# Performance work log

Hardware: AMD Instinct MI355X
Metric: run time of the kernel (lower is better)

Reference implementation:

```python
import jax, jax.numpy as jnp
import numpy as np

B, C, N, T = 16, 32, 1024, 128
R = 10  # low-rank bottleneck of W1/W2


def setup_inputs() -> dict:
    key = jax.random.key(0)
    k1, k2, k3, k4 = jax.random.split(key, 4)
    x = jax.random.normal(k1, (B, C, N, T), dtype=jnp.float32)
    W1 = jax.random.normal(k2, (R, N), dtype=jnp.float32) * 0.05
    W2 = jax.random.normal(k3, (R, N), dtype=jnp.float32) * 0.05
    alpha = jax.random.normal(k4, (C,), dtype=jnp.float32) * 0.1
    return {"x": x, "W1": W1, "W2": W2, "alpha": alpha}


def reference(x, W1, W2, alpha):
    # k = q = einsum('bint,i->btn', x, alpha): contract channels -> [B, T, N]
    k = jnp.einsum('bcnt,c->btn', x, alpha)
    # low-rank bilinear scores: (k @ W1^T) @ (k @ W2^T)^T -> [B, T, T]
    kw1 = jnp.einsum('btn,rn->btr', k, W1)   # [B, T, R]
    qw2 = jnp.einsum('btn,rn->btr', k, W2)   # [B, T, R]
    scores = jnp.einsum('btr,bsr->bts', kw1, qw2)  # [B, T, T]
    att = jax.nn.softmax(scores, axis=-1)
    # weighted sum over time: einsum('bti,bcni->bcnt', att, x)
    return jnp.einsum('bts,bcns->bcnt', att, x)
```

## Files before the change

kernel.cpp:

```cpp
#include <hip/hip_runtime.h>
#include <hip/hip_bf16.h>


#define B_ 16
#define C_ 32
#define N_ 1024
#define T_ 128
#define R_ 10

typedef __bf16 bf16x8 __attribute__((ext_vector_type(8)));
typedef __bf16 bf16x4 __attribute__((ext_vector_type(4)));
typedef float f32x4 __attribute__((ext_vector_type(4)));

__device__ __forceinline__ void lds_barrier() {
    asm volatile("s_waitcnt lgkmcnt(0)" ::: "memory");
    __builtin_amdgcn_s_barrier();
    asm volatile("" ::: "memory");
}

__global__ __launch_bounds__(256) void k_reduce_c(const float* __restrict__ x,
                                                  const float* __restrict__ alpha,
                                                  float* __restrict__ k) {
    int bid = blockIdx.x;
    int b   = bid >> 7;
    int nc  = bid & 127;
    int tid = threadIdx.x;
    int nl  = tid >> 5;
    int lc  = tid & 31;
    int n   = nc * 8 + nl;
    const float4* xb = reinterpret_cast<const float4*>(
        x + ((size_t)(b * C_) * N_ + n) * T_) + lc;
    float4 acc = {0.f, 0.f, 0.f, 0.f};
    #pragma unroll 8
    for (int c = 0; c < C_; ++c) {
        float a = alpha[c];
        float4 v = xb[(size_t)c * (N_ * T_ / 4)];
        acc.x += a * v.x; acc.y += a * v.y; acc.z += a * v.z; acc.w += a * v.w;
    }
    reinterpret_cast<float4*>(k + ((size_t)b * N_ + n) * T_)[lc] = acc;
}

__global__ __launch_bounds__(128) void kw_partial2(const float* __restrict__ k,
                                                   const float* __restrict__ W1,
                                                   const float* __restrict__ W2,
                                                   float* __restrict__ p1,
                                                   float* __restrict__ p2) {
    __shared__ float wl[32][20];
    int bid = blockIdx.x;
    int b   = bid >> 5;
    int ch  = bid & 31;
    int n0  = ch * 32;
    int t   = threadIdx.x;
    for (int i = t; i < 32 * 20; i += 128) {
        int nl = i & 31, q = i >> 5;
        wl[nl][q] = (q < 10) ? W1[q * N_ + n0 + nl] : W2[(q - 10) * N_ + n0 + nl];
    }
    __syncthreads();
    float a1[R_] = {}, a2[R_] = {};
    const float* kb = k + ((size_t)b * N_ + n0) * T_ + t;
    #pragma unroll 2
    for (int g = 0; g < 4; ++g) {
        float kv[8];
        #pragma unroll
        for (int j = 0; j < 8; ++j) kv[j] = kb[(g * 8 + j) * T_];
        #pragma unroll
        for (int j = 0; j < 8; ++j) {
            int nl = g * 8 + j;
            #pragma unroll
            for (int r = 0; r < R_; ++r) {
                a1[r] += kv[j] * wl[nl][r];
                a2[r] += kv[j] * wl[nl][10 + r];
            }
        }
    }
    #pragma unroll
    for (int r = 0; r < R_; ++r) {
        size_t o = (((size_t)b * R_ + r) * 32 + ch) * T_ + t;
        p1[o] = a1[r];
        p2[o] = a2[r];
    }
}

__global__ __launch_bounds__(128) void scores_softmax3(const float* __restrict__ p1,
                                                       const float* __restrict__ p2,
                                                       __bf16* __restrict__ att) {
    __shared__ __align__(16) float kw1s[T_][12];
    __shared__ __align__(16) float kw2s[T_][12];
    __shared__ float sc[T_][T_ + 1];
    int b = blockIdx.x;
    int t = threadIdx.x;
    #pragma unroll
    for (int r = 0; r < R_; ++r) {
        float s1 = 0.f, s2 = 0.f;
        const float* q1 = p1 + (((size_t)b * R_ + r) * 32) * T_ + t;
        const float* q2 = p2 + (((size_t)b * R_ + r) * 32) * T_ + t;
        #pragma unroll 4
        for (int ch = 0; ch < 32; ++ch) { s1 += q1[ch * T_]; s2 += q2[ch * T_]; }
        kw1s[t][r] = s1; kw2s[t][r] = s2;
    }
    __syncthreads();
    float myw[R_];
    #pragma unroll
    for (int r = 0; r < R_; ++r) myw[r] = kw1s[t][r];
    float mx = -1e30f;
    for (int s = 0; s < T_; ++s) {
        float wv[12];
        const float4* qr = reinterpret_cast<const float4*>(&kw2s[s][0]);
        #pragma unroll
        for (int q = 0; q < 3; ++q) *reinterpret_cast<float4*>(&wv[q * 4]) = qr[q];
        float v = 0.f;
        #pragma unroll
        for (int r = 0; r < R_; ++r) v += myw[r] * wv[r];
        sc[t][s] = v;
        mx = fmaxf(mx, v);
    }
    float sum = 0.f;
    for (int s = 0; s < T_; ++s) {
        float e = __expf(sc[t][s] - mx);
        sc[t][s] = e;
        sum += e;
    }
    float inv = 1.0f / sum;
    __bf16* arow = att + ((size_t)b * T_ + t) * T_;
    for (int s8 = 0; s8 < T_; s8 += 8) {
        bf16x8 hv;
        #pragma unroll
        for (int q = 0; q < 8; ++q) hv[q] = (__bf16)(sc[t][s8 + q] * inv);
        *reinterpret_cast<bf16x8*>(arow + s8) = hv;
    }
}

__global__ __launch_bounds__(256, 2) void out_gemm4nt(const float* __restrict__ x,
                                                      const __bf16* __restrict__ att,
                                                      float* __restrict__ out) {
    __shared__ __align__(16) __bf16 attl[T_][T_];
    __shared__ __align__(16) __bf16 xsl[2][64][T_];
    int bid = blockIdx.x;
    int sg  = bid & 3;
    int c   = (bid >> 2) & 31;
    int b   = bid >> 7;
    int tid = threadIdx.x;
    char* attb = (char*)&attl[0][0];
    size_t slab0 = ((size_t)(b * C_ + c) * N_ + (sg * 4) * 64) * T_;

    const uint4* ga = reinterpret_cast<const uint4*>(att + (size_t)b * T_ * T_);
    uint4 ar[8];
    #pragma unroll
    for (int i = 0; i < 8; ++i) ar[i] = ga[i * 256 + tid];
    const f32x4* gx0 = reinterpret_cast<const f32x4*>(x + slab0);
    f32x4 xr[8];
    #pragma unroll
    for (int j = 0; j < 8; ++j) xr[j] = __builtin_nontemporal_load(&gx0[j * 256 + tid]);
    #pragma unroll
    for (int i = 0; i < 8; ++i) {
        int e = i * 256 + tid, row = e >> 4;
        int bc = ((e & 15) * 16) ^ ((row & 7) << 4);
        *reinterpret_cast<uint4*>(attb + row * 256 + bc) = ar[i];
    }
    {
        char* xb0 = (char*)&xsl[0][0][0];
        #pragma unroll
        for (int j = 0; j < 8; ++j) {
            int e = j * 256 + tid, row = e >> 5;
            bf16x4 hv = {(__bf16)xr[j][0], (__bf16)xr[j][1], (__bf16)xr[j][2], (__bf16)xr[j][3]};
            *reinterpret_cast<bf16x4*>(xb0 + row * 256 + (((e & 31) * 8) ^ ((row & 7) << 4))) = hv;
        }
    }
    lds_barrier();

    int wave = tid >> 6, lane = tid & 63;
    int r16 = lane & 15, g = lane >> 4;
    int wt = wave & 1, wn = wave >> 1;
    int swz = (r16 & 7) << 4;

    #pragma unroll
    for (int i = 0; i < 4; ++i) {
        f32x4 xn[8];
        if (i < 3) {
            const f32x4* gxn = reinterpret_cast<const f32x4*>(
                x + slab0 + ((size_t)(i + 1) * 64) * T_);
            #pragma unroll
            for (int j = 0; j < 8; ++j) xn[j] = __builtin_nontemporal_load(&gxn[j * 256 + tid]);
        }
        const char* xbb = (const char*)&xsl[i & 1][0][0];
        f32x4 acc[2][4] = {};
        #pragma unroll
        for (int ks = 0; ks < 4; ++ks) {
            int kc = ks * 64 + g * 16;
            bf16x8 a[4], bx[2];
            #pragma unroll
            for (int tt = 0; tt < 4; ++tt)
                a[tt] = *reinterpret_cast<const bf16x8*>(
                    attb + (wt * 64 + tt * 16 + r16) * 256 + (kc ^ swz));
            #pragma unroll
            for (int nn = 0; nn < 2; ++nn)
                bx[nn] = *reinterpret_cast<const bf16x8*>(
                    xbb + (wn * 32 + nn * 16 + r16) * 256 + (kc ^ swz));
            #pragma unroll
            for (int nn = 0; nn < 2; ++nn)
                #pragma unroll
                for (int tt = 0; tt < 4; ++tt)
                    acc[nn][tt] = __builtin_amdgcn_mfma_f32_16x16x32_bf16(
                        a[tt], bx[nn], acc[nn][tt], 0, 0, 0);
        }
        float* o = out + slab0 + ((size_t)i * 64) * T_;
        #pragma unroll
        for (int nn = 0; nn < 2; ++nn) {
            int n_l = wn * 32 + nn * 16 + r16;
            #pragma unroll
            for (int tt = 0; tt < 4; ++tt)
                __builtin_nontemporal_store(acc[nn][tt],
                    reinterpret_cast<f32x4*>(
                        o + (size_t)n_l * T_ + (wt * 64 + tt * 16 + g * 4)));
        }
        if (i < 3) {
            char* xw = (char*)&xsl[(i + 1) & 1][0][0];
            #pragma unroll
            for (int j = 0; j < 8; ++j) {
                int e = j * 256 + tid, row = e >> 5;
                bf16x4 hv = {(__bf16)xn[j][0], (__bf16)xn[j][1],
                             (__bf16)xn[j][2], (__bf16)xn[j][3]};
                *reinterpret_cast<bf16x4*>(
                    xw + row * 256 + (((e & 31) * 8) ^ ((row & 7) << 4))) = hv;
            }
            lds_barrier();
        }
    }
}

extern "C" void kernel_launch(void* const* d_in, const int* in_sizes, int n_in,
                              void* d_out, int out_size, void* d_ws, size_t ws_size,
                              hipStream_t stream) {
    const float* x     = (const float*)d_in[0];
    const float* W1    = (const float*)d_in[1];
    const float* W2    = (const float*)d_in[2];
    const float* alpha = (const float*)d_in[3];
    float* out = (float*)d_out;

    const size_t KSZ = (size_t)B_ * N_ * T_;
    const size_t PSZ = (size_t)B_ * R_ * 32 * T_;
    float* k    = (float*)d_ws;
    float* p1   = k + KSZ;
    float* p2   = p1 + PSZ;
    __bf16* att = (__bf16*)(p2 + PSZ);

    k_reduce_c     <<<dim3(B_ * (N_ / 8)), dim3(256), 0, stream>>>(x, alpha, k);
    kw_partial2    <<<dim3(B_ * 32),       dim3(128), 0, stream>>>(k, W1, W2, p1, p2);
    scores_softmax3<<<dim3(B_),            dim3(128), 0, stream>>>(p1, p2, att);
    out_gemm4nt    <<<dim3(B_ * C_ * 4),   dim3(256), 0, stream>>>(x, att, out);
}
```

Before: 199.6 us.

## Process full N per block with two-deep register prefetch in output GEMM

The output GEMM kernel now launches one block per (batch, channel) and loops over all 16 N-chunks instead of 4, so the attention tile is loaded into LDS once per block rather than four times. x loads are prefetched two chunks ahead through a pair of register buffers. Nontemporal load/store hints are replaced by plain accesses. Fewer blocks reduce latency hiding across blocks and raise register pressure.

```diff
diff --git a/kernel.cpp b/kernel.cpp
--- a/kernel.cpp
+++ b/kernel.cpp
@@ -130,27 +130,31 @@
     }
 }
 
-__global__ __launch_bounds__(256, 2) void out_gemm4nt(const float* __restrict__ x,
-                                                      const __bf16* __restrict__ att,
-                                                      float* __restrict__ out) {
+__global__ __launch_bounds__(256, 2) void out_gemm9(const float* __restrict__ x,
+                                                    const __bf16* __restrict__ att,
+                                                    float* __restrict__ out) {
     __shared__ __align__(16) __bf16 attl[T_][T_];
     __shared__ __align__(16) __bf16 xsl[2][64][T_];
     int bid = blockIdx.x;
-    int sg  = bid & 3;
-    int c   = (bid >> 2) & 31;
-    int b   = bid >> 7;
+    int c   = bid & 31;
+    int b   = bid >> 5;
     int tid = threadIdx.x;
     char* attb = (char*)&attl[0][0];
-    size_t slab0 = ((size_t)(b * C_ + c) * N_ + (sg * 4) * 64) * T_;
+    size_t base = ((size_t)(b * C_ + c) * N_) * T_;
 
     const uint4* ga = reinterpret_cast<const uint4*>(att + (size_t)b * T_ * T_);
     uint4 ar[8];
     #pragma unroll
     for (int i = 0; i < 8; ++i) ar[i] = ga[i * 256 + tid];
-    const f32x4* gx0 = reinterpret_cast<const f32x4*>(x + slab0);
-    f32x4 xr[8];
-    #pragma unroll
-    for (int j = 0; j < 8; ++j) xr[j] = __builtin_nontemporal_load(&gx0[j * 256 + tid]);
+    f32x4 xs[2][8];
+    {
+        const f32x4* g0 = reinterpret_cast<const f32x4*>(x + base);
+        #pragma unroll
+        for (int j = 0; j < 8; ++j) xs[0][j] = g0[j * 256 + tid];
+        const f32x4* g1 = reinterpret_cast<const f32x4*>(x + base + (size_t)64 * T_);
+        #pragma unroll
+        for (int j = 0; j < 8; ++j) xs[1][j] = g1[j * 256 + tid];
+    }
     #pragma unroll
     for (int i = 0; i < 8; ++i) {
         int e = i * 256 + tid, row = e >> 4;
@@ -158,12 +162,13 @@
         *reinterpret_cast<uint4*>(attb + row * 256 + bc) = ar[i];
     }
     {
-        char* xb0 = (char*)&xsl[0][0][0];
+        char* xw = (char*)&xsl[0][0][0];
         #pragma unroll
         for (int j = 0; j < 8; ++j) {
             int e = j * 256 + tid, row = e >> 5;
-            bf16x4 hv = {(__bf16)xr[j][0], (__bf16)xr[j][1], (__bf16)xr[j][2], (__bf16)xr[j][3]};
-            *reinterpret_cast<bf16x4*>(xb0 + row * 256 + (((e & 31) * 8) ^ ((row & 7) << 4))) = hv;
+            bf16x4 hv = {(__bf16)xs[0][j][0], (__bf16)xs[0][j][1],
+                         (__bf16)xs[0][j][2], (__bf16)xs[0][j][3]};
+            *reinterpret_cast<bf16x4*>(xw + row * 256 + (((e & 31) * 8) ^ ((row & 7) << 4))) = hv;
         }
     }
     lds_barrier();
@@ -174,13 +179,12 @@
     int swz = (r16 & 7) << 4;
 
     #pragma unroll
-    for (int i = 0; i < 4; ++i) {
-        f32x4 xn[8];
-        if (i < 3) {
-            const f32x4* gxn = reinterpret_cast<const f32x4*>(
-                x + slab0 + ((size_t)(i + 1) * 64) * T_);
-            #pragma unroll
-            for (int j = 0; j < 8; ++j) xn[j] = __builtin_nontemporal_load(&gxn[j * 256 + tid]);
+    for (int i = 0; i < 16; ++i) {
+        if (i < 14) {
+            const f32x4* gn = reinterpret_cast<const f32x4*>(
+                x + base + ((size_t)(i + 2) * 64) * T_);
+            #pragma unroll
+            for (int j = 0; j < 8; ++j) xs[i & 1][j] = gn[j * 256 + tid];
         }
         const char* xbb = (const char*)&xsl[i & 1][0][0];
         f32x4 acc[2][4] = {};
@@ -203,23 +207,22 @@
                     acc[nn][tt] = __builtin_amdgcn_mfma_f32_16x16x32_bf16(
                         a[tt], bx[nn], acc[nn][tt], 0, 0, 0);
         }
-        float* o = out + slab0 + ((size_t)i * 64) * T_;
+        float* o = out + base + ((size_t)i * 64) * T_;
         #pragma unroll
         for (int nn = 0; nn < 2; ++nn) {
             int n_l = wn * 32 + nn * 16 + r16;
             #pragma unroll
             for (int tt = 0; tt < 4; ++tt)
-                __builtin_nontemporal_store(acc[nn][tt],
-                    reinterpret_cast<f32x4*>(
-                        o + (size_t)n_l * T_ + (wt * 64 + tt * 16 + g * 4)));
-        }
-        if (i < 3) {
+                *reinterpret_cast<f32x4*>(
+                    o + (size_t)n_l * T_ + (wt * 64 + tt * 16 + g * 4)) = acc[nn][tt];
+        }
+        if (i < 15) {
             char* xw = (char*)&xsl[(i + 1) & 1][0][0];
             #pragma unroll
             for (int j = 0; j < 8; ++j) {
                 int e = j * 256 + tid, row = e >> 5;
-                bf16x4 hv = {(__bf16)xn[j][0], (__bf16)xn[j][1],
-                             (__bf16)xn[j][2], (__bf16)xn[j][3]};
+                bf16x4 hv = {(__bf16)xs[(i + 1) & 1][j][0], (__bf16)xs[(i + 1) & 1][j][1],
+                             (__bf16)xs[(i + 1) & 1][j][2], (__bf16)xs[(i + 1) & 1][j][3]};
                 *reinterpret_cast<bf16x4*>(
                     xw + row * 256 + (((e & 31) * 8) ^ ((row & 7) << 4))) = hv;
             }
@@ -247,5 +250,5 @@
     k_reduce_c     <<<dim3(B_ * (N_ / 8)), dim3(256), 0, stream>>>(x, alpha, k);
     kw_partial2    <<<dim3(B_ * 32),       dim3(128), 0, stream>>>(k, W1, W2, p1, p2);
     scores_softmax3<<<dim3(B_),            dim3(128), 0, stream>>>(p1, p2, att);
-    out_gemm4nt    <<<dim3(B_ * C_ * 4),   dim3(256), 0, stream>>>(x, att, out);
-}
+    out_gemm9      <<<dim3(B_ * C_),       dim3(256), 0, stream>>>(x, att, out);
+}
```

New measurement: 206.8 us. 3.6% more time.

## Read attention fragments directly from global memory and raise occupancy

Applied to the files above, without the earlier changes.

The output GEMM no longer stages the 32KB attention matrix in shared memory. Each wave instead loads its bf16 MFMA A-fragments straight from global memory, where they should hit in cache because many blocks share the same batch's attention. This cuts LDS use and raises launch bounds from 2 to 4 blocks per SM. It also replaces nontemporal loads and stores of x and out with ordinary ones. The cost is repeated global/L2 reads of the attention fragments in every k-step, plus different cache behaviour for the streaming x and out traffic.

```diff
diff --git a/kernel.cpp b/kernel.cpp
--- a/kernel.cpp
+++ b/kernel.cpp
@@ -130,33 +130,28 @@
     }
 }
 
-__global__ __launch_bounds__(256, 2) void out_gemm4nt(const float* __restrict__ x,
-                                                      const __bf16* __restrict__ att,
-                                                      float* __restrict__ out) {
-    __shared__ __align__(16) __bf16 attl[T_][T_];
+__global__ __launch_bounds__(256, 4) void out_gemm10(const float* __restrict__ x,
+                                                     const __bf16* __restrict__ att,
+                                                     float* __restrict__ out) {
     __shared__ __align__(16) __bf16 xsl[2][64][T_];
     int bid = blockIdx.x;
     int sg  = bid & 3;
     int c   = (bid >> 2) & 31;
     int b   = bid >> 7;
     int tid = threadIdx.x;
-    char* attb = (char*)&attl[0][0];
     size_t slab0 = ((size_t)(b * C_ + c) * N_ + (sg * 4) * 64) * T_;
 
-    const uint4* ga = reinterpret_cast<const uint4*>(att + (size_t)b * T_ * T_);
-    uint4 ar[8];
-    #pragma unroll
-    for (int i = 0; i < 8; ++i) ar[i] = ga[i * 256 + tid];
+    int wave = tid >> 6, lane = tid & 63;
+    int r16 = lane & 15, g = lane >> 4;
+    int wt = wave & 1, wn = wave >> 1;
+    int swz = (r16 & 7) << 4;
+    const char* abase = (const char*)(att + (size_t)b * T_ * T_) +
+                        (wt * 64 + r16) * 256 + g * 16;
+
     const f32x4* gx0 = reinterpret_cast<const f32x4*>(x + slab0);
     f32x4 xr[8];
     #pragma unroll
-    for (int j = 0; j < 8; ++j) xr[j] = __builtin_nontemporal_load(&gx0[j * 256 + tid]);
-    #pragma unroll
-    for (int i = 0; i < 8; ++i) {
-        int e = i * 256 + tid, row = e >> 4;
-        int bc = ((e & 15) * 16) ^ ((row & 7) << 4);
-        *reinterpret_cast<uint4*>(attb + row * 256 + bc) = ar[i];
-    }
+    for (int j = 0; j < 8; ++j) xr[j] = gx0[j * 256 + tid];
     {
         char* xb0 = (char*)&xsl[0][0][0];
         #pragma unroll
@@ -167,11 +162,6 @@
         }
     }
     lds_barrier();
-
-    int wave = tid >> 6, lane = tid & 63;
-    int r16 = lane & 15, g = lane >> 4;
-    int wt = wave & 1, wn = wave >> 1;
-    int swz = (r16 & 7) << 4;
 
     #pragma unroll
     for (int i = 0; i < 4; ++i) {
@@ -180,7 +170,7 @@
             const f32x4* gxn = reinterpret_cast<const f32x4*>(
                 x + slab0 + ((size_t)(i + 1) * 64) * T_);
             #pragma unroll
-            for (int j = 0; j < 8; ++j) xn[j] = __builtin_nontemporal_load(&gxn[j * 256 + tid]);
+            for (int j = 0; j < 8; ++j) xn[j] = gxn[j * 256 + tid];
         }
         const char* xbb = (const char*)&xsl[i & 1][0][0];
         f32x4 acc[2][4] = {};
@@ -190,8 +180,7 @@
             bf16x8 a[4], bx[2];
             #pragma unroll
             for (int tt = 0; tt < 4; ++tt)
-                a[tt] = *reinterpret_cast<const bf16x8*>(
-                    attb + (wt * 64 + tt * 16 + r16) * 256 + (kc ^ swz));
+                a[tt] = *reinterpret_cast<const bf16x8*>(abase + tt * 4096 + ks * 64);
             #pragma unroll
             for (int nn = 0; nn < 2; ++nn)
                 bx[nn] = *reinterpret_cast<const bf16x8*>(
@@ -209,9 +198,8 @@
             int n_l = wn * 32 + nn * 16 + r16;
             #pragma unroll
             for (int tt = 0; tt < 4; ++tt)
-                __builtin_nontemporal_store(acc[nn][tt],
-                    reinterpret_cast<f32x4*>(
-                        o + (size_t)n_l * T_ + (wt * 64 + tt * 16 + g * 4)));
+                *reinterpret_cast<f32x4*>(
+                    o + (size_t)n_l * T_ + (wt * 64 + tt * 16 + g * 4)) = acc[nn][tt];
         }
         if (i < 3) {
             char* xw = (char*)&xsl[(i + 1) & 1][0][0];
@@ -247,5 +235,5 @@
     k_reduce_c     <<<dim3(B_ * (N_ / 8)), dim3(256), 0, stream>>>(x, alpha, k);
     kw_partial2    <<<dim3(B_ * 32),       dim3(128), 0, stream>>>(k, W1, W2, p1, p2);
     scores_softmax3<<<dim3(B_),            dim3(128), 0, stream>>>(p1, p2, att);
-    out_gemm4nt    <<<dim3(B_ * C_ * 4),   dim3(256), 0, stream>>>(x, att, out);
-}
+    out_gemm10     <<<dim3(B_ * C_ * 4),   dim3(256), 0, stream>>>(x, att, out);
+}
```

Result: slower. 249.6 us (+25.0%).
